# Kernel tuning notes

Hardware: AMD Instinct MI355X
Metric: run time of the kernel (lower is better)

## Reference

```python
import jax, jax.numpy as jnp
import numpy as np

N_HEADS = 4
ITERS = 3
EPS = 1e-8


def layer_norm(x, g, b, eps=1e-5):
    m = jnp.mean(x, axis=-1, keepdims=True)
    v = jnp.mean((x - m) ** 2, axis=-1, keepdims=True)
    return (x - m) * jax.lax.rsqrt(v + eps) * g + b


def gru_cell(x, h, Wih, Whh, bih, bhh):
    # PyTorch GRUCell semantics. x: [M, kvq], h: [M, dim]
    gi = x @ Wih.T + bih
    gh = h @ Whh.T + bhh
    ir, iz, i_n = jnp.split(gi, 3, axis=-1)
    hr, hz, h_n = jnp.split(gh, 3, axis=-1)
    r = jax.nn.sigmoid(ir + hr)
    z = jax.nn.sigmoid(iz + hz)
    n = jnp.tanh(i_n + r * h_n)
    return (1.0 - z) * n + z * h


def slot_attention(features, slots, Wq, Wk, Wv, g_in, b_in, g_s, b_s, Wih, Whh, bih, bhh):
    b, n, _ = features.shape
    _, ns, dim = slots.shape
    kvq = Wk.shape[0]
    dh = kvq // N_HEADS
    scale = dh ** -0.5
    inp = layer_norm(features, g_in, b_in)
    k = (inp @ Wk.T).reshape(b, n, N_HEADS, dh)
    v = (inp @ Wv.T).reshape(b, n, N_HEADS, dh)
    attn_vis = None
    for _ in range(ITERS):
        slots_prev = slots
        s = layer_norm(slots, g_s, b_s)
        q = (s @ Wq.T).reshape(b, ns, N_HEADS, dh)
        dots = jnp.einsum("bihd,bjhd->bihj", q, k) * scale
        attn = jax.nn.softmax(dots, axis=1)  # competitive softmax over slots
        attn_vis = attn.mean(axis=2)  # [b, ns, n]
        w = attn + EPS
        w = w / jnp.sum(w, axis=-1, keepdims=True)  # weighted mean over features
        upd = jnp.einsum("bjhd,bihj->bihd", v, w).reshape(b, ns, kvq)
        slots = gru_cell(upd.reshape(-1, kvq), slots_prev.reshape(-1, dim),
                         Wih, Whh, bih, bhh).reshape(b, ns, dim)
    return slots, attn_vis


def vq_pool(x, codebook):
    # x: [b, ns, d], codebook: [C, d]
    d2 = (jnp.sum(x ** 2, axis=-1, keepdims=True)
          - 2.0 * jnp.einsum("bnd,cd->bnc", x, codebook)
          + jnp.sum(codebook ** 2, axis=-1))
    idx = jnp.argmin(d2, axis=-1)
    q = codebook[idx]
    commit = jnp.mean((x - jax.lax.stop_gradient(q)) ** 2)
    q = x + jax.lax.stop_gradient(q - x)  # straight-through
    return q, idx, commit


def setup_inputs() -> dict:
    key = jax.random.key(0)
    ks = jax.random.split(key, 16)
    B, N, FD = 32, 1024, 768
    NS, D, KVQ, C = 24, 256, 256, 512
    sc = lambda d: d ** -0.5
    return {
        "features": jax.random.normal(ks[0], (B, N, FD), jnp.float32),
        "conditioning": jax.random.normal(ks[1], (B, NS, D), jnp.float32),
        "Wq": jax.random.normal(ks[2], (KVQ, D), jnp.float32) * sc(D),
        "Wk": jax.random.normal(ks[3], (KVQ, FD), jnp.float32) * sc(FD),
        "Wv": jax.random.normal(ks[4], (KVQ, FD), jnp.float32) * sc(FD),
        "g_in": jnp.ones((FD,), jnp.float32),
        "b_in": jnp.zeros((FD,), jnp.float32),
        "g_s": jnp.ones((D,), jnp.float32),
        "b_s": jnp.zeros((D,), jnp.float32),
        "Wih": jax.random.normal(ks[5], (3 * D, KVQ), jnp.float32) * sc(KVQ),
        "Whh": jax.random.normal(ks[6], (3 * D, D), jnp.float32) * sc(D),
        "bih": jnp.zeros((3 * D,), jnp.float32),
        "bhh": jnp.zeros((3 * D,), jnp.float32),
        "codebook": jax.random.normal(ks[7], (C, D), jnp.float32) * sc(D),
    }


def reference(features, conditioning, Wq, Wk, Wv, g_in, b_in, g_s, b_s,
              Wih, Whh, bih, bhh, codebook):
    sa = lambda f, s: slot_attention(f, s, Wq, Wk, Wv, g_in, b_in, g_s, b_s,
                                     Wih, Whh, bih, bhh)
    slots, pre_attn = sa(features, conditioning)
    q_slots, indices, commit = vq_pool(slots, codebook)
    slots, post_attn = sa(features, q_slots)
    return slots, post_attn, pre_attn, indices, commit
```

## Files before the change

kernel.cpp:

```cpp
#include <hip/hip_runtime.h>
#include <math.h>

#define LB __launch_bounds__(256)

constexpr int BATCH = 32, NFEAT = 1024, FDIM = 768, NSLOT = 24;
constexpr int NH = 4, DH = 64, NITER = 3;
constexpr int MF = BATCH * NFEAT;
constexpr int MS = BATCH * NSLOT;
constexpr float QSCALE = 0.125f;
constexpr float ATTN_EPS = 1e-8f;
constexpr float LNEPS = 1e-5f;

typedef __attribute__((ext_vector_type(8))) short bf16x8;
typedef __attribute__((ext_vector_type(4))) float f32x4;

__device__ __forceinline__ unsigned short f2bf(float x) {
  unsigned u = __float_as_uint(x);
  return (unsigned short)((u + 0x7FFFu + ((u >> 16) & 1u)) >> 16);
}
__device__ __forceinline__ float bf2f(unsigned short h) {
  return __uint_as_float(((unsigned)h) << 16);
}
__device__ __forceinline__ void cvt8(const float4& a, const float4& b, float m, float r,
                                     int4& hi, int4& lo) {
  float v[8] = {a.x, a.y, a.z, a.w, b.x, b.y, b.z, b.w};
  unsigned sh[8], sl[8];
#pragma unroll
  for (int j = 0; j < 8; ++j) {
    float vv = (v[j] - m) * r;
    unsigned short h = f2bf(vv);
    sh[j] = h;
    sl[j] = f2bf(vv - bf2f(h));
  }
  hi = make_int4((int)(sh[0] | (sh[1] << 16)), (int)(sh[2] | (sh[3] << 16)),
                 (int)(sh[4] | (sh[5] << 16)), (int)(sh[6] | (sh[7] << 16)));
  lo = make_int4((int)(sl[0] | (sl[1] << 16)), (int)(sl[2] | (sl[3] << 16)),
                 (int)(sl[4] | (sl[5] << 16)), (int)(sl[6] | (sl[7] << 16)));
}

__device__ __forceinline__ void gll16(const void* g, void* l) {
  __builtin_amdgcn_global_load_lds(
      (const __attribute__((address_space(1))) void*)g,
      (__attribute__((address_space(3))) void*)l, 16, 0, 0);
}

__global__ LB void k_preprow(const float* __restrict__ x, float* __restrict__ stats,
                             const float* __restrict__ Wk, const float* __restrict__ Wv,
                             const float* __restrict__ Wq,
                             const float* __restrict__ g_in, const float* __restrict__ b_in,
                             const float* __restrict__ g_s, const float* __restrict__ b_s,
                             short* __restrict__ Bh_g, short* __restrict__ Bl_g,
                             float* __restrict__ Wgq, float* __restrict__ cconst) {
  const int t = threadIdx.x;
  if (blockIdx.x < MF / 4) {
    const int row = blockIdx.x * 4 + (t >> 6);
    const int lane = t & 63;
    const float* xr = x + (size_t)row * FDIM;
    float s = 0.f, sq = 0.f;
#pragma unroll
    for (int i = 0; i < 3; ++i) {
      float4 v = *(const float4*)(xr + i * 256 + lane * 4);
      s += v.x + v.y + v.z + v.w;
      sq += v.x * v.x + v.y * v.y + v.z * v.z + v.w * v.w;
    }
#pragma unroll
    for (int o = 32; o > 0; o >>= 1) { s += __shfl_down(s, o, 64); sq += __shfl_down(sq, o, 64); }
    if (lane == 0) {
      float m = s / (float)FDIM;
      float var = sq / (float)FDIM - m * m;
      stats[row * 2] = m;
      stats[row * 2 + 1] = 1.f / sqrtf(var + LNEPS);
    }
    return;
  }
  const int r = blockIdx.x - MF / 4;
  float s = 0.f;
  if (r < 512) {
    const float* srcW = (r < 256) ? (Wk + (size_t)r * FDIM) : (Wv + (size_t)(r - 256) * FDIM);
    for (int k = t; k < FDIM; k += 256) {
      float w = srcW[k];
      float wg = w * g_in[k];
      s += b_in[k] * w;
      unsigned short h = f2bf(wg);
      Bh_g[(size_t)r * FDIM + k] = (short)h;
      Bl_g[(size_t)r * FDIM + k] = (short)f2bf(wg - bf2f(h));
    }
  } else {
    const int c = r - 512;
    float w = Wq[(size_t)c * 256 + t];
    Wgq[(size_t)c * 256 + t] = w * g_s[t];
    s = b_s[t] * w;
  }
  __shared__ float red[256];
  red[t] = s; __syncthreads();
  for (int o = 128; o > 0; o >>= 1) { if (t < o) red[t] += red[t + o]; __syncthreads(); }
  if (t == 0) cconst[r] = red[0];
}

__global__ LB void k_mfkv(const float* __restrict__ x, const float* __restrict__ stats,
                          const short* __restrict__ Bh_g, const short* __restrict__ Bl_g,
                          const float* __restrict__ cconst,
                          short* __restrict__ khi, short* __restrict__ klo,
                          float* __restrict__ vout) {
  __shared__ short Ah[2048], Al[2048];
  __shared__ short Bh[2][4096], Bl[2][4096];
  const int t = threadIdx.x;
  const int l = t & 63;
  const int w = t >> 6;
  const int row0 = blockIdx.x * 64;
  const int c0 = blockIdx.y * 128;

  const int sAr = t >> 2;
  const int sl = t & 3;
  const int kqA = sl ^ ((sAr >> 1) & 3);
  const float* pa = x + (size_t)(row0 + sAr) * FDIM + kqA * 8;
  const float mA = stats[(row0 + sAr) * 2], rA = stats[(row0 + sAr) * 2 + 1];
  const int sBr1 = sAr + 64;
  const int kqB1 = sl ^ ((sBr1 >> 1) & 3);
  const short* pkh0 = Bh_g + (size_t)(c0 + sAr) * FDIM + kqA * 8;
  const short* pkh1 = Bh_g + (size_t)(c0 + sBr1) * FDIM + kqB1 * 8;
  const short* pkl0 = Bl_g + (size_t)(c0 + sAr) * FDIM + kqA * 8;
  const short* pkl1 = Bl_g + (size_t)(c0 + sBr1) * FDIM + kqB1 * 8;
  const short* pvh0 = Bh_g + (size_t)(256 + c0 + sAr) * FDIM + kqA * 8;
  const short* pvh1 = Bh_g + (size_t)(256 + c0 + sBr1) * FDIM + kqB1 * 8;
  const short* pvl0 = Bl_g + (size_t)(256 + c0 + sAr) * FDIM + kqA * 8;
  const short* pvl1 = Bl_g + (size_t)(256 + c0 + sBr1) * FDIM + kqB1 * 8;
  const int wbA = t * 16;
  const int wb0 = t * 16, wb1 = (t + 256) * 16;

  const int wm = (w >> 1) * 32, wn = (w & 1) * 64;
  int aoff[2], boff[4];
#pragma unroll
  for (int m = 0; m < 2; ++m) {
    const int ar = wm + m * 16 + (l & 15);
    const int kq = l >> 4;
    aoff[m] = ar * 64 + ((kq ^ ((ar >> 1) & 3)) << 4);
  }
#pragma unroll
  for (int n = 0; n < 4; ++n) {
    const int bc = wn + n * 16 + (l & 15);
    const int kq = l >> 4;
    boff[n] = bc * 64 + ((kq ^ ((bc >> 1) & 3)) << 4);
  }

  f32x4 acc[2][2][4] = {};
  float4 raa = *(const float4*)pa, rab = *(const float4*)(pa + 4);

  for (int s = 0; s < FDIM / 32; ++s) {
    if (s) __syncthreads();
    const int ko = s * 32;
    gll16(pkh0 + ko, (char*)&Bh[0][0] + wb0);
    gll16(pkh1 + ko, (char*)&Bh[0][0] + wb1);
    gll16(pkl0 + ko, (char*)&Bl[0][0] + wb0);
    gll16(pkl1 + ko, (char*)&Bl[0][0] + wb1);
    gll16(pvh0 + ko, (char*)&Bh[1][0] + wb0);
    gll16(pvh1 + ko, (char*)&Bh[1][0] + wb1);
    gll16(pvl0 + ko, (char*)&Bl[1][0] + wb0);
    gll16(pvl1 + ko, (char*)&Bl[1][0] + wb1);
    int4 hi, lo;
    cvt8(raa, rab, mA, rA, hi, lo);
    *(int4*)((char*)Ah + wbA) = hi; *(int4*)((char*)Al + wbA) = lo;
    if (s + 1 < FDIM / 32) {
      raa = *(const float4*)(pa + ko + 32);
      rab = *(const float4*)(pa + ko + 36);
    }
    __syncthreads();
    bf16x8 fah[2], fal[2];
#pragma unroll
    for (int m = 0; m < 2; ++m) {
      fah[m] = *(const bf16x8*)((const char*)Ah + aoff[m]);
      fal[m] = *(const bf16x8*)((const char*)Al + aoff[m]);
    }
#pragma unroll
    for (int kv = 0; kv < 2; ++kv) {
      bf16x8 fbh[4], fbl[4];
#pragma unroll
      for (int n = 0; n < 4; ++n) {
        fbh[n] = *(const bf16x8*)((const char*)&Bh[kv][0] + boff[n]);
        fbl[n] = *(const bf16x8*)((const char*)&Bl[kv][0] + boff[n]);
      }
#pragma unroll
      for (int m = 0; m < 2; ++m)
#pragma unroll
        for (int n = 0; n < 4; ++n) {
          acc[kv][m][n] = __builtin_amdgcn_mfma_f32_16x16x32_bf16(fal[m], fbh[n], acc[kv][m][n], 0, 0, 0);
          acc[kv][m][n] = __builtin_amdgcn_mfma_f32_16x16x32_bf16(fah[m], fbl[n], acc[kv][m][n], 0, 0, 0);
          acc[kv][m][n] = __builtin_amdgcn_mfma_f32_16x16x32_bf16(fah[m], fbh[n], acc[kv][m][n], 0, 0, 0);
        }
    }
  }
#pragma unroll
  for (int m = 0; m < 2; ++m) {
    const int rbase = row0 + wm + m * 16 + ((l >> 4) << 2);
#pragma unroll
    for (int n = 0; n < 4; ++n) {
      const int col = c0 + wn + n * 16 + (l & 15);
      const float cck = cconst[col];
      const float ccv = cconst[256 + col];
#pragma unroll
      for (int r = 0; r < 4; ++r) {
        const float kval = acc[0][m][n][r] + cck;
        const unsigned short h = f2bf(kval);
        khi[(size_t)(rbase + r) * 256 + col] = (short)h;
        klo[(size_t)(rbase + r) * 256 + col] = (short)f2bf(kval - bf2f(h));
        vout[(size_t)(rbase + r) * 256 + col] = acc[1][m][n][r] + ccv;
      }
    }
  }
}

template <bool WRITE_ATTN>
__global__ LB void k_fdots(const float* __restrict__ slots, const float* __restrict__ Wgq,
                           const float* __restrict__ cconst,
                           const short* __restrict__ khi, const short* __restrict__ klo,
                           const float* __restrict__ vmat,
                           float* __restrict__ attn, float* __restrict__ updp,
                           float* __restrict__ ssump) {
  const int blk = blockIdx.x;
  const int jc = blk & 3;
  const int h = (blk >> 2) & 3;
  const int b = blk >> 4;
  const int t = threadIdx.x;
  const int l = t & 63;
  const int w = t >> 6;
  __shared__ float Uat[32 * 256];
  __shared__ short qh[2048], ql[2048];
  __shared__ float vt[DH][DH];
  __shared__ float ssr[NSLOT][8];
  __shared__ float mst[NSLOT], rst[NSLOT];
  if (t < 192) {
    const int r = t >> 3, g = t & 7;
    const float* sr = slots + (size_t)(b * NSLOT + r) * 256 + g * 32;
    float s = 0.f, sq = 0.f;
#pragma unroll
    for (int m4 = 0; m4 < 8; ++m4) {
      float4 v = *(const float4*)(sr + m4 * 4);
      *(float4*)&Uat[r * 256 + g * 32 + m4 * 4] = v;
      s += v.x + v.y + v.z + v.w;
      sq += v.x * v.x + v.y * v.y + v.z * v.z + v.w * v.w;
    }
    s += __shfl_down(s, 4, 8); sq += __shfl_down(sq, 4, 8);
    s += __shfl_down(s, 2, 8); sq += __shfl_down(sq, 2, 8);
    s += __shfl_down(s, 1, 8); sq += __shfl_down(sq, 1, 8);
    if (g == 0) {
      float mm = s * (1.f / 256.f);
      mst[r] = mm;
      rst[r] = 1.f / sqrtf(sq * (1.f / 256.f) - mm * mm + LNEPS);
    }
  }
  __syncthreads();
  for (int lidx = t; lidx < NSLOT * 256; lidx += 256) {
    const int i = lidx >> 8, kk = lidx & 255;
    Uat[i * 256 + kk] = (Uat[i * 256 + kk] - mst[i]) * rst[i];
  }
  __syncthreads();
  {
    const int d = t & 63, ig = t >> 6;
    const float* wrow = Wgq + (size_t)(h * 64 + d) * 256;
    float aq[6] = {};
    for (int k4 = 0; k4 < 256; k4 += 4) {
      const float4 wv = *(const float4*)(wrow + k4);
#pragma unroll
      for (int u = 0; u < 6; ++u) {
        const float4 uv = *(const float4*)&Uat[(ig * 6 + u) * 256 + k4];
        aq[u] += uv.x * wv.x + uv.y * wv.y + uv.z * wv.z + uv.w * wv.w;
      }
    }
    const float qc = cconst[512 + h * 64 + d];
#pragma unroll
    for (int u = 0; u < 6; ++u) {
      const int row = ig * 6 + u;
      const float qv = aq[u] + qc;
      const unsigned short hh = f2bf(qv);
      const unsigned short ll2 = f2bf(qv - bf2f(hh));
      const int slot = row * 8 + ((d >> 3) ^ (row & 7));
      qh[slot * 8 + (d & 7)] = (short)hh;
      ql[slot * 8 + (d & 7)] = (short)ll2;
    }
#pragma unroll
    for (int z = 0; z < 2; ++z) {
      const int e = z * 256 + t;
      const int row = 24 + (e >> 6), dd = e & 63;
      const int slot = row * 8 + ((dd >> 3) ^ (row & 7));
      qh[slot * 8 + (dd & 7)] = 0;
      ql[slot * 8 + (dd & 7)] = 0;
    }
  }
  __syncthreads();
  {
    const short* khb = khi + (size_t)(b * NFEAT + jc * 256) * 256 + h * 64;
    const short* klb = klo + (size_t)(b * NFEAT + jc * 256) * 256 + h * 64;
    f32x4 scc[2][4] = {};
#pragma unroll
    for (int ks = 0; ks < 2; ++ks) {
      bf16x8 ah[2], al[2];
#pragma unroll
      for (int m = 0; m < 2; ++m) {
        const int row = m * 16 + (l & 15);
        const int g = ks * 4 + (l >> 4);
        const int slot = row * 8 + (g ^ (row & 7));
        ah[m] = *(const bf16x8*)&qh[slot * 8];
        al[m] = *(const bf16x8*)&ql[slot * 8];
      }
#pragma unroll
      for (int nl = 0; nl < 4; ++nl) {
        const int nt = w * 4 + nl;
        const size_t boffg = (size_t)(nt * 16 + (l & 15)) * 256 + ks * 32 + (l >> 4) * 8;
        const bf16x8 bh = *(const bf16x8*)(khb + boffg);
        const bf16x8 bl2 = *(const bf16x8*)(klb + boffg);
#pragma unroll
        for (int m = 0; m < 2; ++m) {
          scc[m][nl] = __builtin_amdgcn_mfma_f32_16x16x32_bf16(al[m], bh, scc[m][nl], 0, 0, 0);
          scc[m][nl] = __builtin_amdgcn_mfma_f32_16x16x32_bf16(ah[m], bl2, scc[m][nl], 0, 0, 0);
          scc[m][nl] = __builtin_amdgcn_mfma_f32_16x16x32_bf16(ah[m], bh, scc[m][nl], 0, 0, 0);
        }
      }
    }
#pragma unroll
    for (int m = 0; m < 2; ++m)
#pragma unroll
      for (int nl = 0; nl < 4; ++nl) {
        const int col = (w * 4 + nl) * 16 + (l & 15);
        const int rbase = m * 16 + ((l >> 4) << 2);
#pragma unroll
        for (int r = 0; r < 4; ++r)
          Uat[(rbase + r) * 256 + col] = scc[m][nl][r];
      }
  }
  __syncthreads();
  {
    float acc[NSLOT];
#pragma unroll
    for (int i = 0; i < NSLOT; ++i) acc[i] = Uat[i * 256 + t];
    float mx = -1e30f;
#pragma unroll
    for (int i = 0; i < NSLOT; ++i) { acc[i] *= QSCALE; mx = fmaxf(mx, acc[i]); }
    float s = 0.f;
#pragma unroll
    for (int i = 0; i < NSLOT; ++i) { acc[i] = expf(acc[i] - mx); s += acc[i]; }
    const float inv = 1.f / s;
    float* ab = attn + (size_t)(b * NH + h) * NSLOT * NFEAT + jc * 256 + t;
#pragma unroll
    for (int i = 0; i < NSLOT; ++i) {
      const float wgt = acc[i] * inv;
      if (WRITE_ATTN) ab[(size_t)i * NFEAT] = wgt;
      Uat[i * 256 + t] = wgt + ATTN_EPS;
    }
  }
  __syncthreads();
  if (t < 192) {
    const int i = t >> 3, s8 = t & 7;
    float sp = 0.f;
#pragma unroll
    for (int m = 0; m < 32; ++m) sp += Uat[i * 256 + s8 * 32 + ((m + t) & 31)];
    ssr[i][s8] = sp;
  }
  const int d = t & 63;
  const int ig = t >> 6;
  float acc2[6] = {};
  for (int j0 = 0; j0 < 256; j0 += 64) {
    __syncthreads();
#pragma unroll
    for (int rl = 0; rl < 4; ++rl) {
      const int lidx = rl * 1024 + t * 4;
      const int jj = lidx >> 6, dd = lidx & 63;
      *(float4*)&vt[jj][dd] =
          *(const float4*)(vmat + (size_t)(b * NFEAT + jc * 256 + j0 + jj) * 256 + h * 64 + dd);
    }
    __syncthreads();
#pragma unroll 4
    for (int jj4 = 0; jj4 < 64; jj4 += 4) {
      float4 w4[6];
#pragma unroll
      for (int u = 0; u < 6; ++u) w4[u] = *(const float4*)&Uat[(ig * 6 + u) * 256 + j0 + jj4];
      const float vv0 = vt[jj4 + 0][d];
      const float vv1 = vt[jj4 + 1][d];
      const float vv2 = vt[jj4 + 2][d];
      const float vv3 = vt[jj4 + 3][d];
#pragma unroll
      for (int u = 0; u < 6; ++u) {
        acc2[u] += w4[u].x * vv0;
        acc2[u] += w4[u].y * vv1;
        acc2[u] += w4[u].z * vv2;
        acc2[u] += w4[u].w * vv3;
      }
    }
  }
  __syncthreads();
  if (t < NSLOT) {
    float sp = 0.f;
#pragma unroll
    for (int u = 0; u < 8; ++u) sp += ssr[t][u];
    ssump[((size_t)(b * NH + h) * 4 + jc) * NSLOT + t] = sp;
  }
  float* up = updp + (((size_t)(b * NH + h) * 4 + jc) * NSLOT) * 64;
#pragma unroll
  for (int u = 0; u < 6; ++u) up[(ig * 6 + u) * 64 + d] = acc2[u];
}

template <bool FINAL>
__global__ LB void k_grufin(const float* __restrict__ updp, const float* __restrict__ ssump,
                            const float* __restrict__ sprev,
                            const float* __restrict__ Wih, const float* __restrict__ Whh,
                            const float* __restrict__ bih, const float* __restrict__ bhh,
                            float* __restrict__ snext, float* __restrict__ outs) {
  __shared__ float updt[8][256];
  __shared__ float Bs[3][16][33];
  const int bx = blockIdx.x;
  const int d0 = blockIdx.y * 32;
  const int rows0 = bx * 8;
  const int t = threadIdx.x;
  {
    const int h = t >> 6, d = t & 63;
#pragma unroll
    for (int u = 0; u < 8; ++u) {
      const int row = rows0 + u;
      const int b = row / 24, i = row - b * 24;
      const size_t base = (size_t)(b * 4 + h) * 4;
      float s = 0.f, wsum = 0.f;
#pragma unroll
      for (int jc = 0; jc < 4; ++jc) {
        s += updp[(base + jc) * (NSLOT * 64) + i * 64 + d];
        wsum += ssump[(base + jc) * NSLOT + i];
      }
      updt[u][h * 64 + d] = s / wsum;
    }
  }
  __syncthreads();
  const int r = t >> 5;
  const int dd = t & 31;
  float accR = 0.f, accZ = 0.f, accN = 0.f, accH = 0.f;
  for (int k0 = 0; k0 < 256; k0 += 16) {
    {
      int i = t;
      {
        const int s = i >> 7, rem = i & 127, c = rem >> 2, kq = rem & 3;
        float4 wv = *(const float4*)(Wih + (size_t)(s * 256 + d0 + c) * 256 + k0 + kq * 4);
        Bs[s][kq * 4 + 0][c] = wv.x; Bs[s][kq * 4 + 1][c] = wv.y;
        Bs[s][kq * 4 + 2][c] = wv.z; Bs[s][kq * 4 + 3][c] = wv.w;
      }
      if (t < 128) {
        i = 256 + t;
        const int s = i >> 7, rem = i & 127, c = rem >> 2, kq = rem & 3;
        float4 wv = *(const float4*)(Wih + (size_t)(s * 256 + d0 + c) * 256 + k0 + kq * 4);
        Bs[s][kq * 4 + 0][c] = wv.x; Bs[s][kq * 4 + 1][c] = wv.y;
        Bs[s][kq * 4 + 2][c] = wv.z; Bs[s][kq * 4 + 3][c] = wv.w;
      }
    }
    __syncthreads();
#pragma unroll
    for (int kk = 0; kk < 16; ++kk) {
      const float a = updt[r][k0 + kk];
      accR += a * Bs[0][kk][dd];
      accZ += a * Bs[1][kk][dd];
      accN += a * Bs[2][kk][dd];
    }
    __syncthreads();
  }
  {
    const int rr2 = t >> 5, c0 = (t & 31) * 8;
    const float* sp = sprev + (size_t)(rows0 + rr2) * 256 + c0;
    *(float4*)&updt[rr2][c0] = *(const float4*)sp;
    *(float4*)&updt[rr2][c0 + 4] = *(const float4*)(sp + 4);
  }
  __syncthreads();
  for (int k0 = 0; k0 < 256; k0 += 16) {
    {
      int i = t;
      {
        const int s = i >> 7, rem = i & 127, c = rem >> 2, kq = rem & 3;
        float4 wv = *(const float4*)(Whh + (size_t)(s * 256 + d0 + c) * 256 + k0 + kq * 4);
        Bs[s][kq * 4 + 0][c] = wv.x; Bs[s][kq * 4 + 1][c] = wv.y;
        Bs[s][kq * 4 + 2][c] = wv.z; Bs[s][kq * 4 + 3][c] = wv.w;
      }
      if (t < 128) {
        i = 256 + t;
        const int s = i >> 7, rem = i & 127, c = rem >> 2, kq = rem & 3;
        float4 wv = *(const float4*)(Whh + (size_t)(s * 256 + d0 + c) * 256 + k0 + kq * 4);
        Bs[s][kq * 4 + 0][c] = wv.x; Bs[s][kq * 4 + 1][c] = wv.y;
        Bs[s][kq * 4 + 2][c] = wv.z; Bs[s][kq * 4 + 3][c] = wv.w;
      }
    }
    __syncthreads();
#pragma unroll
    for (int kk = 0; kk < 16; ++kk) {
      const float a = updt[r][k0 + kk];
      accR += a * Bs[0][kk][dd];
      accZ += a * Bs[1][kk][dd];
      accH += a * Bs[2][kk][dd];
    }
    __syncthreads();
  }
  const int row = rows0 + r;
  const int c = d0 + dd;
  const float hp = updt[r][c];
  const float rr = 1.f / (1.f + expf(-(accR + bih[c] + bhh[c])));
  const float zz = 1.f / (1.f + expf(-(accZ + bih[256 + c] + bhh[256 + c])));
  const float nn = tanhf(accN + bih[512 + c] + rr * (accH + bhh[512 + c]));
  const float o = (1.f - zz) * nn + zz * hp;
  snext[(size_t)row * 256 + c] = o;
  if (FINAL) outs[(size_t)row * 256 + c] = o;
}

__global__ LB void k_attnvis(const float* __restrict__ attn, float* __restrict__ out) {
  const int idx = blockIdx.x * 256 + threadIdx.x;
  const int j = idx & 1023;
  const int rem = idx >> 10;
  const int i = rem % NSLOT;
  const int b = rem / NSLOT;
  float s = 0.f;
#pragma unroll
  for (int h = 0; h < NH; ++h)
    s += attn[(size_t)((b * NH + h) * NSLOT + i) * NFEAT + j];
  out[idx] = 0.25f * s;
}

__global__ LB void k_vqvis(float* __restrict__ slots, const float* __restrict__ cb,
                           const float* __restrict__ attn,
                           float* __restrict__ idx_out, float* __restrict__ bestd2,
                           float* __restrict__ vis_out) {
  const int t = threadIdx.x;
  if (blockIdx.x >= MS) {
    const int idx = (blockIdx.x - MS) * 256 + t;
    const int j = idx & 1023;
    const int rem = idx >> 10;
    const int i = rem % NSLOT;
    const int b = rem / NSLOT;
    float s = 0.f;
#pragma unroll
    for (int h = 0; h < NH; ++h)
      s += attn[(size_t)((b * NH + h) * NSLOT + i) * NFEAT + j];
    vis_out[idx] = 0.25f * s;
    return;
  }
  const int r = blockIdx.x;
  __shared__ float xs[256];
  __shared__ float red[256];
  __shared__ float rv[256];
  __shared__ int ri[256];
  xs[t] = slots[(size_t)r * 256 + t];
  __syncthreads();
  red[t] = xs[t] * xs[t]; __syncthreads();
  for (int o = 128; o > 0; o >>= 1) { if (t < o) red[t] += red[t + o]; __syncthreads(); }
  const float x2 = red[0];
  float best = 1e30f; int bidx = 0;
#pragma unroll
  for (int cset = 0; cset < 2; ++cset) {
    const int c = cset * 256 + t;
    const float* cr = cb + (size_t)c * 256;
    float xc = 0.f, cc = 0.f;
    for (int dd = 0; dd < 256; dd += 4) {
      float4 cv = *(const float4*)(cr + dd);
      xc += xs[dd] * cv.x + xs[dd + 1] * cv.y + xs[dd + 2] * cv.z + xs[dd + 3] * cv.w;
      cc += cv.x * cv.x + cv.y * cv.y + cv.z * cv.z + cv.w * cv.w;
    }
    float d2 = x2 - 2.f * xc + cc;
    if (d2 < best) { best = d2; bidx = c; }
  }
  rv[t] = best; ri[t] = bidx; __syncthreads();
  for (int o = 128; o > 0; o >>= 1) {
    if (t < o) {
      if (rv[t + o] < rv[t] || (rv[t + o] == rv[t] && ri[t + o] < ri[t])) {
        rv[t] = rv[t + o]; ri[t] = ri[t + o];
      }
    }
    __syncthreads();
  }
  const int wi = ri[0];
  const float cval = cb[(size_t)wi * 256 + t];
  const float diff = xs[t] - cval;
  red[t] = diff * diff; __syncthreads();
  for (int o = 128; o > 0; o >>= 1) { if (t < o) red[t] += red[t + o]; __syncthreads(); }
  if (t == 0) { idx_out[r] = (float)wi; bestd2[r] = red[0]; }
  slots[(size_t)r * 256 + t] = cval;
}

__global__ LB void k_commit(const float* __restrict__ bestd2, float* __restrict__ out) {
  const int t = threadIdx.x;
  __shared__ float red[256];
  float s = 0.f;
  for (int i = t; i < MS; i += 256) s += bestd2[i];
  red[t] = s; __syncthreads();
  for (int o = 128; o > 0; o >>= 1) { if (t < o) red[t] += red[t + o]; __syncthreads(); }
  if (t == 0) out[0] = red[0] / (float)(MS * 256);
}

extern "C" void kernel_launch(void* const* d_in, const int* in_sizes, int n_in,
                              void* d_out, int out_size, void* d_ws, size_t ws_size,
                              hipStream_t stream) {
  const float* features = (const float*)d_in[0];
  const float* cond = (const float*)d_in[1];
  const float* Wq = (const float*)d_in[2];
  const float* Wk = (const float*)d_in[3];
  const float* Wv = (const float*)d_in[4];
  const float* g_in = (const float*)d_in[5];
  const float* b_in = (const float*)d_in[6];
  const float* g_s = (const float*)d_in[7];
  const float* b_s = (const float*)d_in[8];
  const float* Wih = (const float*)d_in[9];
  const float* Whh = (const float*)d_in[10];
  const float* bih = (const float*)d_in[11];
  const float* bhh = (const float*)d_in[12];
  const float* cb = (const float*)d_in[13];
  float* out = (float*)d_out;

  char* wsb = (char*)d_ws;
  short* Bh_g = (short*)wsb; wsb += (size_t)512 * FDIM * 2;
  short* Bl_g = (short*)wsb; wsb += (size_t)512 * FDIM * 2;
  short* khi = (short*)wsb; wsb += (size_t)MF * 256 * 2;
  short* klo = (short*)wsb; wsb += (size_t)MF * 256 * 2;
  float* ws = (float*)wsb;
  float* stats = ws;  ws += 2 * MF;
  float* vbuf = ws;   ws += (size_t)MF * 256;
  float* attn = ws;   ws += (size_t)BATCH * NH * NSLOT * NFEAT;
  float* sbufA = ws;  ws += (size_t)MS * 256;
  float* sbufB = ws;  ws += (size_t)MS * 256;
  float* updp = ws;   ws += (size_t)512 * NSLOT * 64;
  float* ssump = ws;  ws += (size_t)512 * NSLOT;
  float* Wgq = ws;    ws += 256 * 256;
  float* cconst = ws; ws += 768;
  float* bestd2 = ws; ws += MS;

  float* out_slots = out;
  float* out_post = out + 196608;
  float* out_pre = out + 196608 + 786432;
  float* out_idx = out + 196608 + 786432 * 2;
  float* out_commit = out_idx + 768;

  k_preprow<<<MF / 4 + 768, 256, 0, stream>>>(features, stats, Wk, Wv, Wq, g_in, b_in,
                                              g_s, b_s, Bh_g, Bl_g, Wgq, cconst);
  k_mfkv<<<dim3(MF / 64, 2), 256, 0, stream>>>(features, stats, Bh_g, Bl_g, cconst,
                                               khi, klo, vbuf);

  const float* scur = cond;
  float* bufs[2] = {sbufA, sbufB};
  int nb = 0;
  for (int call = 0; call < 2; ++call) {
    for (int it = 0; it < NITER; ++it) {
      float* snxt = bufs[nb]; nb ^= 1;
      if (it == NITER - 1)
        k_fdots<true><<<512, 256, 0, stream>>>(scur, Wgq, cconst, khi, klo, vbuf,
                                               attn, updp, ssump);
      else
        k_fdots<false><<<512, 256, 0, stream>>>(scur, Wgq, cconst, khi, klo, vbuf,
                                                attn, updp, ssump);
      if (call == 1 && it == NITER - 1)
        k_grufin<true><<<dim3(MS / 8, 8), 256, 0, stream>>>(updp, ssump, scur, Wih, Whh,
                                                            bih, bhh, snxt, out_slots);
      else
        k_grufin<false><<<dim3(MS / 8, 8), 256, 0, stream>>>(updp, ssump, scur, Wih, Whh,
                                                             bih, bhh, snxt, out_slots);
      scur = snxt;
    }
    if (call == 0) {
      k_vqvis<<<MS + BATCH * NSLOT * NFEAT / 256, 256, 0, stream>>>(
          (float*)scur, cb, attn, out_idx, bestd2, out_pre);
      k_commit<<<1, 256, 0, stream>>>(bestd2, out_commit);
    } else {
      k_attnvis<<<BATCH * NSLOT * NFEAT / 256, 256, 0, stream>>>(attn, out_post);
    }
  }
}
```

Measured before the change: 642.3 us.

## Use split-bf16 MFMA for query projection and attention-weighted V update

Moves the per-iteration q projection and the attn·V reduction in k_fdots from scalar FP32 loops onto 3-pass split-bf16 MFMA. To support this, V is now stored transposed as hi/lo bf16 halves per batch and head, and the gamma-scaled Wq as hi/lo bf16. Row sums become wave shuffles instead of a separate LDS pass. The cost is extra conversion work and scattered transposed stores in k_mfkv, plus a small precision change from split-bf16 arithmetic.

```diff
diff --git a/kernel.cpp b/kernel.cpp
--- a/kernel.cpp
+++ b/kernel.cpp
@@ -50,7 +50,8 @@
                              const float* __restrict__ g_in, const float* __restrict__ b_in,
                              const float* __restrict__ g_s, const float* __restrict__ b_s,
                              short* __restrict__ Bh_g, short* __restrict__ Bl_g,
-                             float* __restrict__ Wgq, float* __restrict__ cconst) {
+                             short* __restrict__ Wgqh, short* __restrict__ Wgql,
+                             float* __restrict__ cconst) {
   const int t = threadIdx.x;
   if (blockIdx.x < MF / 4) {
     const int row = blockIdx.x * 4 + (t >> 6);
@@ -88,7 +89,10 @@
   } else {
     const int c = r - 512;
     float w = Wq[(size_t)c * 256 + t];
-    Wgq[(size_t)c * 256 + t] = w * g_s[t];
+    float wg = w * g_s[t];
+    unsigned short hh = f2bf(wg);
+    Wgqh[(size_t)c * 256 + t] = (short)hh;
+    Wgql[(size_t)c * 256 + t] = (short)f2bf(wg - bf2f(hh));
     s = b_s[t] * w;
   }
   __shared__ float red[256];
@@ -101,7 +105,7 @@
                           const short* __restrict__ Bh_g, const short* __restrict__ Bl_g,
                           const float* __restrict__ cconst,
                           short* __restrict__ khi, short* __restrict__ klo,
-                          float* __restrict__ vout) {
+                          short* __restrict__ vThi, short* __restrict__ vTlo) {
   __shared__ short Ah[2048], Al[2048];
   __shared__ short Bh[2][4096], Bl[2][4096];
   const int t = threadIdx.x;
@@ -189,31 +193,40 @@
         }
     }
   }
+  const int b_blk = row0 >> 10;
+  const int jbase = row0 & 1023;
 #pragma unroll
   for (int m = 0; m < 2; ++m) {
-    const int rbase = row0 + wm + m * 16 + ((l >> 4) << 2);
+    const int rloc = wm + m * 16 + ((l >> 4) << 2);
+    const int rbase = row0 + rloc;
 #pragma unroll
     for (int n = 0; n < 4; ++n) {
       const int col = c0 + wn + n * 16 + (l & 15);
       const float cck = cconst[col];
       const float ccv = cconst[256 + col];
+      const int hh2 = col >> 6, dh = col & 63;
+      const size_t vrow = ((size_t)(b_blk * 4 + hh2) * 64 + dh) * 1024;
 #pragma unroll
       for (int r = 0; r < 4; ++r) {
         const float kval = acc[0][m][n][r] + cck;
         const unsigned short h = f2bf(kval);
         khi[(size_t)(rbase + r) * 256 + col] = (short)h;
         klo[(size_t)(rbase + r) * 256 + col] = (short)f2bf(kval - bf2f(h));
-        vout[(size_t)(rbase + r) * 256 + col] = acc[1][m][n][r] + ccv;
+        const float vval = acc[1][m][n][r] + ccv;
+        const unsigned short hv = f2bf(vval);
+        vThi[vrow + jbase + rloc + r] = (short)hv;
+        vTlo[vrow + jbase + rloc + r] = (short)f2bf(vval - bf2f(hv));
       }
     }
   }
 }
 
 template <bool WRITE_ATTN>
-__global__ LB void k_fdots(const float* __restrict__ slots, const float* __restrict__ Wgq,
+__global__ LB void k_fdots(const float* __restrict__ slots,
+                           const short* __restrict__ Wgqh, const short* __restrict__ Wgql,
                            const float* __restrict__ cconst,
                            const short* __restrict__ khi, const short* __restrict__ klo,
-                           const float* __restrict__ vmat,
+                           const short* __restrict__ vThi, const short* __restrict__ vTlo,
                            float* __restrict__ attn, float* __restrict__ updp,
                            float* __restrict__ ssump) {
   const int blk = blockIdx.x;
@@ -223,11 +236,13 @@
   const int t = threadIdx.x;
   const int l = t & 63;
   const int w = t >> 6;
-  __shared__ float Uat[32 * 256];
+  __shared__ float sc[24 * 256];
+  __shared__ short sh_[32 * 256];
+  __shared__ short sl_[32 * 256];
   __shared__ short qh[2048], ql[2048];
-  __shared__ float vt[DH][DH];
-  __shared__ float ssr[NSLOT][8];
+  __shared__ float part[4][NSLOT];
   __shared__ float mst[NSLOT], rst[NSLOT];
+
   if (t < 192) {
     const int r = t >> 3, g = t & 7;
     const float* sr = slots + (size_t)(b * NSLOT + r) * 256 + g * 32;
@@ -235,7 +250,7 @@
 #pragma unroll
     for (int m4 = 0; m4 < 8; ++m4) {
       float4 v = *(const float4*)(sr + m4 * 4);
-      *(float4*)&Uat[r * 256 + g * 32 + m4 * 4] = v;
+      *(float4*)&sc[r * 256 + g * 32 + m4 * 4] = v;
       s += v.x + v.y + v.z + v.w;
       sq += v.x * v.x + v.y * v.y + v.z * v.z + v.w * v.w;
     }
@@ -249,42 +264,51 @@
     }
   }
   __syncthreads();
-  for (int lidx = t; lidx < NSLOT * 256; lidx += 256) {
-    const int i = lidx >> 8, kk = lidx & 255;
-    Uat[i * 256 + kk] = (Uat[i * 256 + kk] - mst[i]) * rst[i];
+#pragma unroll 4
+  for (int i = 0; i < NSLOT; ++i) {
+    const float v = (sc[i * 256 + t] - mst[i]) * rst[i];
+    const unsigned short hh = f2bf(v);
+    const int slot = i * 32 + ((t >> 3) ^ (i & 31));
+    sh_[slot * 8 + (t & 7)] = (short)hh;
+    sl_[slot * 8 + (t & 7)] = (short)f2bf(v - bf2f(hh));
   }
   __syncthreads();
   {
-    const int d = t & 63, ig = t >> 6;
-    const float* wrow = Wgq + (size_t)(h * 64 + d) * 256;
-    float aq[6] = {};
-    for (int k4 = 0; k4 < 256; k4 += 4) {
-      const float4 wv = *(const float4*)(wrow + k4);
-#pragma unroll
-      for (int u = 0; u < 6; ++u) {
-        const float4 uv = *(const float4*)&Uat[(ig * 6 + u) * 256 + k4];
-        aq[u] += uv.x * wv.x + uv.y * wv.y + uv.z * wv.z + uv.w * wv.w;
-      }
-    }
+    f32x4 qacc[2] = {};
+#pragma unroll
+    for (int ks = 0; ks < 8; ++ks) {
+      bf16x8 ah[2], al[2];
+#pragma unroll
+      for (int m = 0; m < 2; ++m) {
+        const int row = m * 16 + (l & 15);
+        const int g = ks * 4 + (l >> 4);
+        const int slot = row * 32 + (g ^ (row & 31));
+        ah[m] = *(const bf16x8*)&sh_[slot * 8];
+        al[m] = *(const bf16x8*)&sl_[slot * 8];
+      }
+      const size_t brow = (size_t)(h * 64 + w * 16 + (l & 15)) * 256 + ks * 32 + (l >> 4) * 8;
+      const bf16x8 bh = *(const bf16x8*)(Wgqh + brow);
+      const bf16x8 bl2 = *(const bf16x8*)(Wgql + brow);
+#pragma unroll
+      for (int m = 0; m < 2; ++m) {
+        qacc[m] = __builtin_amdgcn_mfma_f32_16x16x32_bf16(al[m], bh, qacc[m], 0, 0, 0);
+        qacc[m] = __builtin_amdgcn_mfma_f32_16x16x32_bf16(ah[m], bl2, qacc[m], 0, 0, 0);
+        qacc[m] = __builtin_amdgcn_mfma_f32_16x16x32_bf16(ah[m], bh, qacc[m], 0, 0, 0);
+      }
+    }
+    const int d = w * 16 + (l & 15);
     const float qc = cconst[512 + h * 64 + d];
 #pragma unroll
-    for (int u = 0; u < 6; ++u) {
-      const int row = ig * 6 + u;
-      const float qv = aq[u] + qc;
-      const unsigned short hh = f2bf(qv);
-      const unsigned short ll2 = f2bf(qv - bf2f(hh));
-      const int slot = row * 8 + ((d >> 3) ^ (row & 7));
-      qh[slot * 8 + (d & 7)] = (short)hh;
-      ql[slot * 8 + (d & 7)] = (short)ll2;
-    }
-#pragma unroll
-    for (int z = 0; z < 2; ++z) {
-      const int e = z * 256 + t;
-      const int row = 24 + (e >> 6), dd = e & 63;
-      const int slot = row * 8 + ((dd >> 3) ^ (row & 7));
-      qh[slot * 8 + (dd & 7)] = 0;
-      ql[slot * 8 + (dd & 7)] = 0;
-    }
+    for (int m = 0; m < 2; ++m)
+#pragma unroll
+      for (int r = 0; r < 4; ++r) {
+        const int row = m * 16 + (l >> 4) * 4 + r;
+        const float qv = qacc[m][r] + qc;
+        const unsigned short hh = f2bf(qv);
+        const int slot = row * 8 + ((d >> 3) ^ (row & 7));
+        qh[slot * 8 + (d & 7)] = (short)hh;
+        ql[slot * 8 + (d & 7)] = (short)f2bf(qv - bf2f(hh));
+      }
   }
   __syncthreads();
   {
@@ -324,14 +348,14 @@
         const int rbase = m * 16 + ((l >> 4) << 2);
 #pragma unroll
         for (int r = 0; r < 4; ++r)
-          Uat[(rbase + r) * 256 + col] = scc[m][nl][r];
+          if (rbase + r < 24) sc[(rbase + r) * 256 + col] = scc[m][nl][r];
       }
   }
   __syncthreads();
   {
     float acc[NSLOT];
 #pragma unroll
-    for (int i = 0; i < NSLOT; ++i) acc[i] = Uat[i * 256 + t];
+    for (int i = 0; i < NSLOT; ++i) acc[i] = sc[i * 256 + t];
     float mx = -1e30f;
 #pragma unroll
     for (int i = 0; i < NSLOT; ++i) { acc[i] *= QSCALE; mx = fmaxf(mx, acc[i]); }
@@ -344,58 +368,59 @@
     for (int i = 0; i < NSLOT; ++i) {
       const float wgt = acc[i] * inv;
       if (WRITE_ATTN) ab[(size_t)i * NFEAT] = wgt;
-      Uat[i * 256 + t] = wgt + ATTN_EPS;
-    }
-  }
-  __syncthreads();
-  if (t < 192) {
-    const int i = t >> 3, s8 = t & 7;
-    float sp = 0.f;
-#pragma unroll
-    for (int m = 0; m < 32; ++m) sp += Uat[i * 256 + s8 * 32 + ((m + t) & 31)];
-    ssr[i][s8] = sp;
-  }
-  const int d = t & 63;
-  const int ig = t >> 6;
-  float acc2[6] = {};
-  for (int j0 = 0; j0 < 256; j0 += 64) {
-    __syncthreads();
-#pragma unroll
-    for (int rl = 0; rl < 4; ++rl) {
-      const int lidx = rl * 1024 + t * 4;
-      const int jj = lidx >> 6, dd = lidx & 63;
-      *(float4*)&vt[jj][dd] =
-          *(const float4*)(vmat + (size_t)(b * NFEAT + jc * 256 + j0 + jj) * 256 + h * 64 + dd);
-    }
-    __syncthreads();
-#pragma unroll 4
-    for (int jj4 = 0; jj4 < 64; jj4 += 4) {
-      float4 w4[6];
-#pragma unroll
-      for (int u = 0; u < 6; ++u) w4[u] = *(const float4*)&Uat[(ig * 6 + u) * 256 + j0 + jj4];
-      const float vv0 = vt[jj4 + 0][d];
-      const float vv1 = vt[jj4 + 1][d];
-      const float vv2 = vt[jj4 + 2][d];
-      const float vv3 = vt[jj4 + 3][d];
-#pragma unroll
-      for (int u = 0; u < 6; ++u) {
-        acc2[u] += w4[u].x * vv0;
-        acc2[u] += w4[u].y * vv1;
-        acc2[u] += w4[u].z * vv2;
-        acc2[u] += w4[u].w * vv3;
-      }
-    }
-  }
-  __syncthreads();
-  if (t < NSLOT) {
-    float sp = 0.f;
-#pragma unroll
-    for (int u = 0; u < 8; ++u) sp += ssr[t][u];
-    ssump[((size_t)(b * NH + h) * 4 + jc) * NSLOT + t] = sp;
-  }
-  float* up = updp + (((size_t)(b * NH + h) * 4 + jc) * NSLOT) * 64;
-#pragma unroll
-  for (int u = 0; u < 6; ++u) up[(ig * 6 + u) * 64 + d] = acc2[u];
+      const float ae = wgt + ATTN_EPS;
+      acc[i] = ae;
+      const unsigned short hh = f2bf(ae);
+      const int slot = i * 32 + ((t >> 3) ^ (i & 31));
+      sh_[slot * 8 + (t & 7)] = (short)hh;
+      sl_[slot * 8 + (t & 7)] = (short)f2bf(ae - bf2f(hh));
+    }
+#pragma unroll
+    for (int i = 0; i < NSLOT; ++i) {
+      float rs = acc[i];
+#pragma unroll
+      for (int o = 32; o > 0; o >>= 1) rs += __shfl_down(rs, o, 64);
+      if (l == 0) part[w][i] = rs;
+    }
+  }
+  __syncthreads();
+  {
+    f32x4 pacc[2] = {};
+#pragma unroll
+    for (int ks = 0; ks < 8; ++ks) {
+      bf16x8 ah[2], al[2];
+#pragma unroll
+      for (int m = 0; m < 2; ++m) {
+        const int row = m * 16 + (l & 15);
+        const int g = ks * 4 + (l >> 4);
+        const int slot = row * 32 + (g ^ (row & 31));
+        ah[m] = *(const bf16x8*)&sh_[slot * 8];
+        al[m] = *(const bf16x8*)&sl_[slot * 8];
+      }
+      const size_t brow = ((size_t)(b * 4 + h) * 64 + w * 16 + (l & 15)) * 1024 +
+                          jc * 256 + ks * 32 + (l >> 4) * 8;
+      const bf16x8 bh = *(const bf16x8*)(vThi + brow);
+      const bf16x8 bl2 = *(const bf16x8*)(vTlo + brow);
+#pragma unroll
+      for (int m = 0; m < 2; ++m) {
+        pacc[m] = __builtin_amdgcn_mfma_f32_16x16x32_bf16(al[m], bh, pacc[m], 0, 0, 0);
+        pacc[m] = __builtin_amdgcn_mfma_f32_16x16x32_bf16(ah[m], bl2, pacc[m], 0, 0, 0);
+        pacc[m] = __builtin_amdgcn_mfma_f32_16x16x32_bf16(ah[m], bh, pacc[m], 0, 0, 0);
+      }
+    }
+    const int d = w * 16 + (l & 15);
+    float* up = updp + (size_t)((b * 4 + h) * 4 + jc) * NSLOT * 64;
+#pragma unroll
+    for (int m = 0; m < 2; ++m)
+#pragma unroll
+      for (int r = 0; r < 4; ++r) {
+        const int row = m * 16 + (l >> 4) * 4 + r;
+        if (row < 24) up[row * 64 + d] = pacc[m][r];
+      }
+  }
+  if (t < NSLOT)
+    ssump[((size_t)(b * 4 + h) * 4 + jc) * NSLOT + t] =
+        part[0][t] + part[1][t] + part[2][t] + part[3][t];
 }
 
 template <bool FINAL>
@@ -609,15 +634,17 @@
   short* Bl_g = (short*)wsb; wsb += (size_t)512 * FDIM * 2;
   short* khi = (short*)wsb; wsb += (size_t)MF * 256 * 2;
   short* klo = (short*)wsb; wsb += (size_t)MF * 256 * 2;
+  short* vThi = (short*)wsb; wsb += (size_t)MF * 256 * 2;
+  short* vTlo = (short*)wsb; wsb += (size_t)MF * 256 * 2;
+  short* Wgqh = (short*)wsb; wsb += (size_t)256 * 256 * 2;
+  short* Wgql = (short*)wsb; wsb += (size_t)256 * 256 * 2;
   float* ws = (float*)wsb;
   float* stats = ws;  ws += 2 * MF;
-  float* vbuf = ws;   ws += (size_t)MF * 256;
   float* attn = ws;   ws += (size_t)BATCH * NH * NSLOT * NFEAT;
   float* sbufA = ws;  ws += (size_t)MS * 256;
   float* sbufB = ws;  ws += (size_t)MS * 256;
   float* updp = ws;   ws += (size_t)512 * NSLOT * 64;
   float* ssump = ws;  ws += (size_t)512 * NSLOT;
-  float* Wgq = ws;    ws += 256 * 256;
   float* cconst = ws; ws += 768;
   float* bestd2 = ws; ws += MS;
 
@@ -628,9 +655,9 @@
   float* out_commit = out_idx + 768;
 
   k_preprow<<<MF / 4 + 768, 256, 0, stream>>>(features, stats, Wk, Wv, Wq, g_in, b_in,
-                                              g_s, b_s, Bh_g, Bl_g, Wgq, cconst);
+                                              g_s, b_s, Bh_g, Bl_g, Wgqh, Wgql, cconst);
   k_mfkv<<<dim3(MF / 64, 2), 256, 0, stream>>>(features, stats, Bh_g, Bl_g, cconst,
-                                               khi, klo, vbuf);
+                                               khi, klo, vThi, vTlo);
 
   const float* scur = cond;
   float* bufs[2] = {sbufA, sbufB};
@@ -639,11 +666,11 @@
     for (int it = 0; it < NITER; ++it) {
       float* snxt = bufs[nb]; nb ^= 1;
       if (it == NITER - 1)
-        k_fdots<true><<<512, 256, 0, stream>>>(scur, Wgq, cconst, khi, klo, vbuf,
-                                               attn, updp, ssump);
+        k_fdots<true><<<512, 256, 0, stream>>>(scur, Wgqh, Wgql, cconst, khi, klo,
+                                               vThi, vTlo, attn, updp, ssump);
       else
-        k_fdots<false><<<512, 256, 0, stream>>>(scur, Wgq, cconst, khi, klo, vbuf,
-                                                attn, updp, ssump);
+        k_fdots<false><<<512, 256, 0, stream>>>(scur, Wgqh, Wgql, cconst, khi, klo,
+                                                vThi, vTlo, attn, updp, ssump);
       if (call == 1 && it == NITER - 1)
         k_grufin<true><<<dim3(MS / 8, 8), 256, 0, stream>>>(updp, ssump, scur, Wih, Whh,
                                                             bih, bhh, snxt, out_slots);
```

Measured after the change: 557.7 us. 1.15x faster.
